# Kernel optimization log

Measured on AMD Instinct MI355X. Metric: run time of the kernel, lower is better.

## Reference

```python
import jax, jax.numpy as jnp
import numpy as np

B, S, E = 1, 8192, 1024

def setup_inputs() -> dict:
    key = jax.random.key(0)
    ks = jax.random.split(key, 7)
    scale = 1.0 / np.sqrt(E)
    q = jax.random.normal(ks[0], (B, S, E), dtype=jnp.float32)
    Wq = jax.random.uniform(ks[1], (E, E), jnp.float32, -scale, scale)
    bq = jax.random.uniform(ks[2], (E,), jnp.float32, -scale, scale)
    Wk = jax.random.uniform(ks[3], (E, E), jnp.float32, -scale, scale)
    bk = jax.random.uniform(ks[4], (E,), jnp.float32, -scale, scale)
    Wv = jax.random.uniform(ks[5], (E, E), jnp.float32, -scale, scale)
    bv = jax.random.uniform(ks[6], (E,), jnp.float32, -scale, scale)
    return {"q": q, "Wq": Wq, "bq": bq, "Wk": Wk, "bk": bk, "Wv": Wv, "bv": bv}

def reference(q, Wq, bq, Wk, bk, Wv, bv):
    # k and v default to q in the original module
    Q = jnp.einsum('bse,fe->bsf', q, Wq) + bq          # [B,S,E]
    K = jnp.einsum('bse,fe->bsf', q, Wk) + bk          # [B,S,E]
    V = jnp.einsum('bse,fe->bsf', q, Wv) + bv          # [B,S,E]
    weights = jax.nn.softmax(K, axis=1)                # softmax over sequence dim
    # sum over seq -> [B,E], then sum over E keepdim -> [B,1] (faithful to source)
    weighted_context = jnp.sum(weights * V, axis=1).sum(axis=1, keepdims=True)
    Y = jax.nn.sigmoid(Q) * weighted_context           # broadcast (valid since B==1)
    return Y
```

## Files before the change

### kernel.cpp

```cpp
#include <hip/hip_runtime.h>
#include <hip/hip_bf16.h>
#include <stdint.h>

typedef __bf16 bf16_t;
typedef __bf16 bf16x8 __attribute__((ext_vector_type(8)));
typedef float f32x4 __attribute__((ext_vector_type(4)));

#define NKT 16

__device__ __forceinline__ void gload_lds16(const void* g, void* l) {
  using gptr_t = const __attribute__((address_space(1))) void*;
  using lptr_t = __attribute__((address_space(3))) void*;
  gptr_t gp = (gptr_t)(uintptr_t)g;
  lptr_t lp = (lptr_t)(uint32_t)(uintptr_t)l;
  __builtin_amdgcn_global_load_lds(gp, lp, 16, 0, 0);
}

__device__ __forceinline__ bf16x8 cvt8v(const float* __restrict__ src, int i8) {
  const float4* s = reinterpret_cast<const float4*>(src) + (size_t)i8 * 2;
  float4 a = s[0], b = s[1];
  bf16x8 o;
  o[0] = (bf16_t)a.x; o[1] = (bf16_t)a.y; o[2] = (bf16_t)a.z; o[3] = (bf16_t)a.w;
  o[4] = (bf16_t)b.x; o[5] = (bf16_t)b.y; o[6] = (bf16_t)b.z; o[7] = (bf16_t)b.w;
  return o;
}

__global__ __launch_bounds__(256) void cvt_all(const float* __restrict__ q,
                                               const float* __restrict__ Wk,
                                               const float* __restrict__ Wv,
                                               const float* __restrict__ Wq,
                                               const float* __restrict__ bk,
                                               const float* __restrict__ bv,
                                               bf16_t* __restrict__ qb,
                                               bf16_t* __restrict__ Wkv,
                                               bf16_t* __restrict__ Wqb,
                                               float* __restrict__ bkv) {
  const int b = blockIdx.x;
  const int t = threadIdx.x;
  if (b < 4096) {
    int i = b * 256 + t;
    *reinterpret_cast<bf16x8*>(qb + (size_t)i * 8) = cvt8v(q, i);
  } else if (b < 4608) {
    int i = (b - 4096) * 256 + t;
    int j = i >> 7, c8 = i & 127;
    *reinterpret_cast<bf16x8*>(Wkv + (size_t)j * 2048 + c8 * 8) = cvt8v(Wk, i);
  } else if (b < 5120) {
    int i = (b - 4608) * 256 + t;
    int j = i >> 7, c8 = i & 127;
    *reinterpret_cast<bf16x8*>(Wkv + (size_t)j * 2048 + 1024 + c8 * 8) = cvt8v(Wv, i);
  } else if (b < 5632) {
    int i = (b - 5120) * 256 + t;
    *reinterpret_cast<bf16x8*>(Wqb + (size_t)i * 8) = cvt8v(Wq, i);
  } else {
#pragma unroll
    for (int u = 0; u < 4; ++u) {
      int j = t * 4 + u;
      bkv[2 * j] = bk[j];
      bkv[2 * j + 1] = bv[j];
    }
  }
}

__global__ __launch_bounds__(512, 1) void gemm_kv8(const bf16_t* __restrict__ A,
                                                   const bf16_t* __restrict__ Bkv,
                                                   const float* __restrict__ bkv,
                                                   float* __restrict__ pden,
                                                   float* __restrict__ pnum) {
  __shared__ bf16_t lA[2 * 256 * 64];
  __shared__ bf16_t lB[2 * 256 * 64];
  __shared__ float sD[2][128];
  __shared__ float sN[2][128];

  const int tid = threadIdx.x;
  const int w = tid >> 6, l = tid & 63;
  const int wr = w >> 2, wc = w & 3;
  const int swz = (blockIdx.x & 7) * 32 + (blockIdx.x >> 3);
  const int bx = swz & 7, by = swz >> 3;
  const int m0 = by * 256, n0 = bx * 256;

  const int rl3 = l >> 3;
  const int scol = ((l & 7) ^ rl3) * 8;
  const int fr = l & 15, fg = l >> 4, sw = l & 7;

  const bf16_t* Ab = A + (size_t)(m0 + w * 8 + rl3) * 1024 + scol;
  const bf16_t* Bb = Bkv + (size_t)(n0 + w * 8 + rl3) * 1024 + scol;

  f32x4 acc[8][4];
#pragma unroll
  for (int m = 0; m < 8; ++m)
#pragma unroll
    for (int n = 0; n < 4; ++n) acc[m][n] = (f32x4){0.f, 0.f, 0.f, 0.f};

#define STAGE_A(kt, h, r, slot)                                              \
  gload_lds16(Ab + (size_t)((h) * 128 + (r) * 64) * 1024 + (kt) * 64,        \
              &lA[(slot) * 16384 + ((h) * 128 + (r) * 64 + w * 8) * 64])
#define STAGE_B(kt, h, r, slot)                                              \
  gload_lds16(Bb + (size_t)((h) * 128 + (r) * 64) * 1024 + (kt) * 64,        \
              &lB[(slot) * 16384 + ((h) * 128 + (r) * 64 + w * 8) * 64])
#define RD_A(mm, ks) \
  (*reinterpret_cast<const bf16x8*>(&lA[aBase + ((mm) * 16 + fr) * 64 + ((((ks) * 4) + fg) ^ sw) * 8]))
#define RD_B(nn, ks) \
  (*reinterpret_cast<const bf16x8*>(&lB[bBase + ((nn) * 16 + fr) * 64 + ((((ks) * 4) + fg) ^ sw) * 8]))

  STAGE_A(0, 0, 0, 0); STAGE_A(0, 0, 1, 0); STAGE_A(0, 1, 0, 0); STAGE_A(0, 1, 1, 0);
  STAGE_B(0, 0, 0, 0); STAGE_B(0, 0, 1, 0); STAGE_B(0, 1, 0, 0); STAGE_B(0, 1, 1, 0);

#pragma unroll 1
  for (int T = 0; T < NKT; ++T) {
    const int slot = T & 1, ns = slot ^ 1;
    const bool pf = (T + 1) < NKT;
    if (pf) { STAGE_A(T + 1, 0, 0, ns); STAGE_A(T + 1, 0, 1, ns); }
    if (pf) asm volatile("s_waitcnt vmcnt(2)" ::: "memory");
    else    asm volatile("s_waitcnt vmcnt(0)" ::: "memory");
    __builtin_amdgcn_s_barrier();
    __builtin_amdgcn_sched_barrier(0);

    const int aBase = slot * 16384 + wr * 8192;
    const int bBase = slot * 16384 + wc * 4096;
    bf16x8 af[4], bfv[4];
#pragma unroll
    for (int n = 0; n < 4; ++n) bfv[n] = RD_B(n, 0);
#pragma unroll
    for (int m = 0; m < 4; ++m) af[m] = RD_A(m, 0);
    if (pf) { STAGE_A(T + 1, 1, 0, ns); STAGE_A(T + 1, 1, 1, ns); }
    __builtin_amdgcn_s_setprio(1);
#pragma unroll
    for (int m = 0; m < 4; ++m)
#pragma unroll
      for (int n = 0; n < 4; ++n)
        acc[m][n] = __builtin_amdgcn_mfma_f32_16x16x32_bf16(af[m], bfv[n], acc[m][n], 0, 0, 0);
    __builtin_amdgcn_s_setprio(0);
    __builtin_amdgcn_s_barrier();
    __builtin_amdgcn_sched_barrier(0);
#pragma unroll
    for (int m = 0; m < 4; ++m) af[m] = RD_A(m + 4, 0);
    if (pf) { STAGE_B(T + 1, 0, 0, ns); STAGE_B(T + 1, 0, 1, ns); }
    __builtin_amdgcn_s_setprio(1);
#pragma unroll
    for (int m = 0; m < 4; ++m)
#pragma unroll
      for (int n = 0; n < 4; ++n)
        acc[m + 4][n] = __builtin_amdgcn_mfma_f32_16x16x32_bf16(af[m], bfv[n], acc[m + 4][n], 0, 0, 0);
    __builtin_amdgcn_s_setprio(0);
    __builtin_amdgcn_s_barrier();
    __builtin_amdgcn_sched_barrier(0);
#pragma unroll
    for (int n = 0; n < 4; ++n) bfv[n] = RD_B(n, 1);
#pragma unroll
    for (int m = 0; m < 4; ++m) af[m] = RD_A(m, 1);
    if (pf) { STAGE_B(T + 1, 1, 0, ns); STAGE_B(T + 1, 1, 1, ns); }
    __builtin_amdgcn_s_setprio(1);
#pragma unroll
    for (int m = 0; m < 4; ++m)
#pragma unroll
      for (int n = 0; n < 4; ++n)
        acc[m][n] = __builtin_amdgcn_mfma_f32_16x16x32_bf16(af[m], bfv[n], acc[m][n], 0, 0, 0);
    __builtin_amdgcn_s_setprio(0);
    __builtin_amdgcn_s_barrier();
    __builtin_amdgcn_sched_barrier(0);
#pragma unroll
    for (int m = 0; m < 4; ++m) af[m] = RD_A(m + 4, 1);
    __builtin_amdgcn_s_setprio(1);
#pragma unroll
    for (int m = 0; m < 4; ++m)
#pragma unroll
      for (int n = 0; n < 4; ++n)
        acc[m + 4][n] = __builtin_amdgcn_mfma_f32_16x16x32_bf16(af[m], bfv[n], acc[m + 4][n], 0, 0, 0);
    __builtin_amdgcn_s_setprio(0);
    __builtin_amdgcn_s_barrier();
    __builtin_amdgcn_sched_barrier(0);
  }

  float dpn[4] = {0.f, 0.f, 0.f, 0.f};
  float npn[4] = {0.f, 0.f, 0.f, 0.f};
#pragma unroll
  for (int n = 0; n < 4; ++n) {
    const int col = n0 + wc * 64 + n * 16 + fr;
    const float bc = bkv[col];
#pragma unroll
    for (int m = 0; m < 8; ++m)
#pragma unroll
      for (int r = 0; r < 4; ++r) {
        float x = acc[m][n][r] + bc;
        float xp = __shfl_xor(x, 1);
        float e = __expf(x);
        dpn[n] += e;
        npn[n] += e * xp;
      }
    dpn[n] += __shfl_xor(dpn[n], 16); dpn[n] += __shfl_xor(dpn[n], 32);
    npn[n] += __shfl_xor(npn[n], 16); npn[n] += __shfl_xor(npn[n], 32);
  }
  if (l < 16 && (l & 1) == 0) {
#pragma unroll
    for (int n = 0; n < 4; ++n) {
      sD[wr][wc * 32 + n * 8 + (l >> 1)] = dpn[n];
      sN[wr][wc * 32 + n * 8 + (l >> 1)] = npn[n];
    }
  }
  __syncthreads();
  if (tid < 128) {
    pden[(size_t)by * 1024 + bx * 128 + tid] = sD[0][tid] + sD[1][tid];
    pnum[(size_t)by * 1024 + bx * 128 + tid] = sN[0][tid] + sN[1][tid];
  }
#undef STAGE_A
#undef STAGE_B
#undef RD_A
#undef RD_B
}

__global__ __launch_bounds__(1024) void finalize(const float* __restrict__ pden,
                                                 const float* __restrict__ pnum,
                                                 float* __restrict__ cval) {
  const int t = threadIdx.x;
  float d = 0.f, nm = 0.f;
  for (int b = 0; b < 32; ++b) {
    d += pden[b * 1024 + t];
    nm += pnum[b * 1024 + t];
  }
  float val = nm / d;
  __shared__ float red[1024];
  red[t] = val;
  __syncthreads();
  for (int s = 512; s > 0; s >>= 1) {
    if (t < s) red[t] += red[t + s];
    __syncthreads();
  }
  if (t == 0) cval[0] = red[0];
}

__global__ __launch_bounds__(512, 1) void gemm_q8(const bf16_t* __restrict__ A,
                                                  const bf16_t* __restrict__ Bq,
                                                  const float* __restrict__ bias,
                                                  const float* __restrict__ cptr,
                                                  float* __restrict__ C) {
  __shared__ bf16_t lA[2 * 256 * 64];
  __shared__ bf16_t lB[2 * 128 * 64];

  const int tid = threadIdx.x;
  const int w = tid >> 6, l = tid & 63;
  const int wr = w >> 1, wc = w & 1;
  const int swz = (blockIdx.x & 7) * 32 + (blockIdx.x >> 3);
  const int bx = swz & 7, by = swz >> 3;
  const int m0 = by * 256, n0 = bx * 128;

  const int rl3 = l >> 3;
  const int scol = ((l & 7) ^ rl3) * 8;
  const int fr = l & 15, fg = l >> 4, sw = l & 7;

  const bf16_t* Ab = A + (size_t)(m0 + w * 8 + rl3) * 1024 + scol;
  const bf16_t* Bb = Bq + (size_t)(n0 + w * 8 + rl3) * 1024 + scol;

  f32x4 acc[4][4];
#pragma unroll
  for (int m = 0; m < 4; ++m)
#pragma unroll
    for (int n = 0; n < 4; ++n) acc[m][n] = (f32x4){0.f, 0.f, 0.f, 0.f};

#define STAGE_A(kt, h, r, slot)                                              \
  gload_lds16(Ab + (size_t)((h) * 128 + (r) * 64) * 1024 + (kt) * 64,        \
              &lA[(slot) * 16384 + ((h) * 128 + (r) * 64 + w * 8) * 64])
#define STAGE_B(kt, h, slot)                                                 \
  gload_lds16(Bb + (size_t)((h) * 64) * 1024 + (kt) * 64,                    \
              &lB[(slot) * 8192 + ((h) * 64 + w * 8) * 64])
#define RD_A(mm, ks) \
  (*reinterpret_cast<const bf16x8*>(&lA[aBase + ((mm) * 16 + fr) * 64 + ((((ks) * 4) + fg) ^ sw) * 8]))
#define RD_B(nn, ks) \
  (*reinterpret_cast<const bf16x8*>(&lB[bBase + ((nn) * 16 + fr) * 64 + ((((ks) * 4) + fg) ^ sw) * 8]))

  STAGE_A(0, 0, 0, 0); STAGE_A(0, 0, 1, 0); STAGE_A(0, 1, 0, 0); STAGE_A(0, 1, 1, 0);
  STAGE_B(0, 0, 0); STAGE_B(0, 1, 0);

#pragma unroll 1
  for (int T = 0; T < NKT; ++T) {
    const int slot = T & 1, ns = slot ^ 1;
    const bool pf = (T + 1) < NKT;
    if (pf) { STAGE_A(T + 1, 0, 0, ns); STAGE_A(T + 1, 0, 1, ns); }
    if (pf) asm volatile("s_waitcnt vmcnt(2)" ::: "memory");
    else    asm volatile("s_waitcnt vmcnt(0)" ::: "memory");
    __builtin_amdgcn_s_barrier();
    __builtin_amdgcn_sched_barrier(0);

    const int aBase = slot * 16384 + wr * 4096;
    const int bBase = slot * 8192 + wc * 4096;
    bf16x8 af[2], bfv[4];
#pragma unroll
    for (int n = 0; n < 4; ++n) bfv[n] = RD_B(n, 0);
    af[0] = RD_A(0, 0); af[1] = RD_A(1, 0);
    if (pf) { STAGE_A(T + 1, 1, 0, ns); STAGE_A(T + 1, 1, 1, ns); }
    __builtin_amdgcn_s_setprio(1);
#pragma unroll
    for (int m = 0; m < 2; ++m)
#pragma unroll
      for (int n = 0; n < 4; ++n)
        acc[m][n] = __builtin_amdgcn_mfma_f32_16x16x32_bf16(af[m], bfv[n], acc[m][n], 0, 0, 0);
    __builtin_amdgcn_s_setprio(0);
    __builtin_amdgcn_s_barrier();
    __builtin_amdgcn_sched_barrier(0);
    af[0] = RD_A(2, 0); af[1] = RD_A(3, 0);
    if (pf) STAGE_B(T + 1, 0, ns);
    __builtin_amdgcn_s_setprio(1);
#pragma unroll
    for (int m = 0; m < 2; ++m)
#pragma unroll
      for (int n = 0; n < 4; ++n)
        acc[m + 2][n] = __builtin_amdgcn_mfma_f32_16x16x32_bf16(af[m], bfv[n], acc[m + 2][n], 0, 0, 0);
    __builtin_amdgcn_s_setprio(0);
    __builtin_amdgcn_s_barrier();
    __builtin_amdgcn_sched_barrier(0);
#pragma unroll
    for (int n = 0; n < 4; ++n) bfv[n] = RD_B(n, 1);
    af[0] = RD_A(0, 1); af[1] = RD_A(1, 1);
    if (pf) STAGE_B(T + 1, 1, ns);
    __builtin_amdgcn_s_setprio(1);
#pragma unroll
    for (int m = 0; m < 2; ++m)
#pragma unroll
      for (int n = 0; n < 4; ++n)
        acc[m][n] = __builtin_amdgcn_mfma_f32_16x16x32_bf16(af[m], bfv[n], acc[m][n], 0, 0, 0);
    __builtin_amdgcn_s_setprio(0);
    __builtin_amdgcn_s_barrier();
    __builtin_amdgcn_sched_barrier(0);
    af[0] = RD_A(2, 1); af[1] = RD_A(3, 1);
    __builtin_amdgcn_s_setprio(1);
#pragma unroll
    for (int m = 0; m < 2; ++m)
#pragma unroll
      for (int n = 0; n < 4; ++n)
        acc[m + 2][n] = __builtin_amdgcn_mfma_f32_16x16x32_bf16(af[m], bfv[n], acc[m + 2][n], 0, 0, 0);
    __builtin_amdgcn_s_setprio(0);
    __builtin_amdgcn_s_barrier();
    __builtin_amdgcn_sched_barrier(0);
  }

  const float cv = cptr[0];
#pragma unroll
  for (int n = 0; n < 4; ++n) {
    const int col = n0 + wc * 64 + n * 16 + fr;
    const float bs = bias[col];
#pragma unroll
    for (int m = 0; m < 4; ++m) {
      const int row = m0 + wr * 64 + m * 16 + fg * 4;
#pragma unroll
      for (int r = 0; r < 4; ++r) {
        float v = acc[m][n][r] + bs;
        v = cv / (1.f + __expf(-v));
        C[(size_t)(row + r) * 1024 + col] = v;
      }
    }
  }
#undef STAGE_A
#undef STAGE_B
#undef RD_A
#undef RD_B
}

extern "C" void kernel_launch(void* const* d_in, const int* in_sizes, int n_in,
                              void* d_out, int out_size, void* d_ws, size_t ws_size,
                              hipStream_t stream) {
  const float* q = (const float*)d_in[0];
  const float* Wq = (const float*)d_in[1];
  const float* bq = (const float*)d_in[2];
  const float* Wk = (const float*)d_in[3];
  const float* bk = (const float*)d_in[4];
  const float* Wv = (const float*)d_in[5];
  const float* bv = (const float*)d_in[6];
  float* out = (float*)d_out;

  char* ws = (char*)d_ws;
  bf16_t* qb = (bf16_t*)ws;
  bf16_t* Wkv = (bf16_t*)(ws + (size_t)16 * 1024 * 1024);
  bf16_t* Wqb = (bf16_t*)(ws + (size_t)20 * 1024 * 1024);
  float* bkv = (float*)(ws + (size_t)22 * 1024 * 1024);
  float* pden = (float*)(ws + (size_t)23 * 1024 * 1024);
  float* pnum = (float*)(ws + (size_t)23 * 1024 * 1024 + 131072);
  float* cval = (float*)(ws + (size_t)23 * 1024 * 1024 + 262144);

  cvt_all<<<5633, 256, 0, stream>>>(q, Wk, Wv, Wq, bk, bv, qb, Wkv, Wqb, bkv);
  gemm_kv8<<<256, 512, 0, stream>>>(qb, Wkv, bkv, pden, pnum);
  finalize<<<1, 1024, 0, stream>>>(pden, pnum, cval);
  gemm_q8<<<256, 512, 0, stream>>>(qb, Wqb, bq, cval, out);
}
```

Before: 77.84 us.

## Fuse KV GEMM, finalize and Q GEMM into one persistent kernel with grid barrier

Merges the KV GEMM, the single-block finalize reduction and the Q GEMM into one kernel of 256 blocks. Each block publishes its softmax partials, increments an atomic counter, computes its Q tile while other blocks finish, then spins until all 256 have arrived and reduces the partials itself. This removes two kernel launches and the serial one-block finalize, and hides the barrier wait behind the Q GEMM. In exchange it relies on all 256 blocks being co-resident, adds a memset, and has every block redundantly read all partials; the spin is capped, so a missed arrival would give wrong results rather than hang.

```diff
diff --git a/kernel.cpp b/kernel.cpp
--- a/kernel.cpp
+++ b/kernel.cpp
@@ -61,35 +61,44 @@
   }
 }
 
-__global__ __launch_bounds__(512, 1) void gemm_kv8(const bf16_t* __restrict__ A,
+__global__ __launch_bounds__(512, 1) void aft_mega(const bf16_t* __restrict__ A,
                                                    const bf16_t* __restrict__ Bkv,
+                                                   const bf16_t* __restrict__ Bq,
                                                    const float* __restrict__ bkv,
+                                                   const float* __restrict__ bq,
                                                    float* __restrict__ pden,
-                                                   float* __restrict__ pnum) {
+                                                   float* __restrict__ pnum,
+                                                   int* __restrict__ bar,
+                                                   float* __restrict__ out) {
   __shared__ bf16_t lA[2 * 256 * 64];
   __shared__ bf16_t lB[2 * 256 * 64];
   __shared__ float sD[2][128];
   __shared__ float sN[2][128];
+  __shared__ float red[512];
 
   const int tid = threadIdx.x;
   const int w = tid >> 6, l = tid & 63;
-  const int wr = w >> 2, wc = w & 3;
   const int swz = (blockIdx.x & 7) * 32 + (blockIdx.x >> 3);
   const int bx = swz & 7, by = swz >> 3;
-  const int m0 = by * 256, n0 = bx * 256;
+  const int m0 = by * 256;
 
   const int rl3 = l >> 3;
   const int scol = ((l & 7) ^ rl3) * 8;
   const int fr = l & 15, fg = l >> 4, sw = l & 7;
 
-  const bf16_t* Ab = A + (size_t)(m0 + w * 8 + rl3) * 1024 + scol;
-  const bf16_t* Bb = Bkv + (size_t)(n0 + w * 8 + rl3) * 1024 + scol;
-
-  f32x4 acc[8][4];
-#pragma unroll
-  for (int m = 0; m < 8; ++m)
-#pragma unroll
-    for (int n = 0; n < 4; ++n) acc[m][n] = (f32x4){0.f, 0.f, 0.f, 0.f};
+  const bf16_t* Abase = A + (size_t)(m0 + w * 8 + rl3) * 1024 + scol;
+
+  {
+    const int kwr = w >> 2, kwc = w & 3;
+    const int n0 = bx * 256;
+    const bf16_t* Ab = Abase;
+    const bf16_t* Bb = Bkv + (size_t)(n0 + w * 8 + rl3) * 1024 + scol;
+
+    f32x4 acc[8][4];
+#pragma unroll
+    for (int m = 0; m < 8; ++m)
+#pragma unroll
+      for (int n = 0; n < 4; ++n) acc[m][n] = (f32x4){0.f, 0.f, 0.f, 0.f};
 
 #define STAGE_A(kt, h, r, slot)                                              \
   gload_lds16(Ab + (size_t)((h) * 128 + (r) * 64) * 1024 + (kt) * 64,        \
@@ -102,159 +111,128 @@
 #define RD_B(nn, ks) \
   (*reinterpret_cast<const bf16x8*>(&lB[bBase + ((nn) * 16 + fr) * 64 + ((((ks) * 4) + fg) ^ sw) * 8]))
 
-  STAGE_A(0, 0, 0, 0); STAGE_A(0, 0, 1, 0); STAGE_A(0, 1, 0, 0); STAGE_A(0, 1, 1, 0);
-  STAGE_B(0, 0, 0, 0); STAGE_B(0, 0, 1, 0); STAGE_B(0, 1, 0, 0); STAGE_B(0, 1, 1, 0);
+    STAGE_A(0, 0, 0, 0); STAGE_A(0, 0, 1, 0); STAGE_A(0, 1, 0, 0); STAGE_A(0, 1, 1, 0);
+    STAGE_B(0, 0, 0, 0); STAGE_B(0, 0, 1, 0); STAGE_B(0, 1, 0, 0); STAGE_B(0, 1, 1, 0);
 
 #pragma unroll 1
-  for (int T = 0; T < NKT; ++T) {
-    const int slot = T & 1, ns = slot ^ 1;
-    const bool pf = (T + 1) < NKT;
-    if (pf) { STAGE_A(T + 1, 0, 0, ns); STAGE_A(T + 1, 0, 1, ns); }
-    if (pf) asm volatile("s_waitcnt vmcnt(2)" ::: "memory");
-    else    asm volatile("s_waitcnt vmcnt(0)" ::: "memory");
-    __builtin_amdgcn_s_barrier();
-    __builtin_amdgcn_sched_barrier(0);
-
-    const int aBase = slot * 16384 + wr * 8192;
-    const int bBase = slot * 16384 + wc * 4096;
-    bf16x8 af[4], bfv[4];
-#pragma unroll
-    for (int n = 0; n < 4; ++n) bfv[n] = RD_B(n, 0);
-#pragma unroll
-    for (int m = 0; m < 4; ++m) af[m] = RD_A(m, 0);
-    if (pf) { STAGE_A(T + 1, 1, 0, ns); STAGE_A(T + 1, 1, 1, ns); }
-    __builtin_amdgcn_s_setprio(1);
-#pragma unroll
-    for (int m = 0; m < 4; ++m)
-#pragma unroll
-      for (int n = 0; n < 4; ++n)
-        acc[m][n] = __builtin_amdgcn_mfma_f32_16x16x32_bf16(af[m], bfv[n], acc[m][n], 0, 0, 0);
-    __builtin_amdgcn_s_setprio(0);
-    __builtin_amdgcn_s_barrier();
-    __builtin_amdgcn_sched_barrier(0);
-#pragma unroll
-    for (int m = 0; m < 4; ++m) af[m] = RD_A(m + 4, 0);
-    if (pf) { STAGE_B(T + 1, 0, 0, ns); STAGE_B(T + 1, 0, 1, ns); }
-    __builtin_amdgcn_s_setprio(1);
-#pragma unroll
-    for (int m = 0; m < 4; ++m)
-#pragma unroll
-      for (int n = 0; n < 4; ++n)
-        acc[m + 4][n] = __builtin_amdgcn_mfma_f32_16x16x32_bf16(af[m], bfv[n], acc[m + 4][n], 0, 0, 0);
-    __builtin_amdgcn_s_setprio(0);
-    __builtin_amdgcn_s_barrier();
-    __builtin_amdgcn_sched_barrier(0);
-#pragma unroll
-    for (int n = 0; n < 4; ++n) bfv[n] = RD_B(n, 1);
-#pragma unroll
-    for (int m = 0; m < 4; ++m) af[m] = RD_A(m, 1);
-    if (pf) { STAGE_B(T + 1, 1, 0, ns); STAGE_B(T + 1, 1, 1, ns); }
-    __builtin_amdgcn_s_setprio(1);
-#pragma unroll
-    for (int m = 0; m < 4; ++m)
-#pragma unroll
-      for (int n = 0; n < 4; ++n)
-        acc[m][n] = __builtin_amdgcn_mfma_f32_16x16x32_bf16(af[m], bfv[n], acc[m][n], 0, 0, 0);
-    __builtin_amdgcn_s_setprio(0);
-    __builtin_amdgcn_s_barrier();
-    __builtin_amdgcn_sched_barrier(0);
-#pragma unroll
-    for (int m = 0; m < 4; ++m) af[m] = RD_A(m + 4, 1);
-    __builtin_amdgcn_s_setprio(1);
-#pragma unroll
-    for (int m = 0; m < 4; ++m)
-#pragma unroll
-      for (int n = 0; n < 4; ++n)
-        acc[m + 4][n] = __builtin_amdgcn_mfma_f32_16x16x32_bf16(af[m], bfv[n], acc[m + 4][n], 0, 0, 0);
-    __builtin_amdgcn_s_setprio(0);
-    __builtin_amdgcn_s_barrier();
-    __builtin_amdgcn_sched_barrier(0);
-  }
-
-  float dpn[4] = {0.f, 0.f, 0.f, 0.f};
-  float npn[4] = {0.f, 0.f, 0.f, 0.f};
-#pragma unroll
-  for (int n = 0; n < 4; ++n) {
-    const int col = n0 + wc * 64 + n * 16 + fr;
-    const float bc = bkv[col];
-#pragma unroll
-    for (int m = 0; m < 8; ++m)
-#pragma unroll
-      for (int r = 0; r < 4; ++r) {
-        float x = acc[m][n][r] + bc;
-        float xp = __shfl_xor(x, 1);
-        float e = __expf(x);
-        dpn[n] += e;
-        npn[n] += e * xp;
-      }
-    dpn[n] += __shfl_xor(dpn[n], 16); dpn[n] += __shfl_xor(dpn[n], 32);
-    npn[n] += __shfl_xor(npn[n], 16); npn[n] += __shfl_xor(npn[n], 32);
-  }
-  if (l < 16 && (l & 1) == 0) {
-#pragma unroll
-    for (int n = 0; n < 4; ++n) {
-      sD[wr][wc * 32 + n * 8 + (l >> 1)] = dpn[n];
-      sN[wr][wc * 32 + n * 8 + (l >> 1)] = npn[n];
-    }
-  }
-  __syncthreads();
-  if (tid < 128) {
-    pden[(size_t)by * 1024 + bx * 128 + tid] = sD[0][tid] + sD[1][tid];
-    pnum[(size_t)by * 1024 + bx * 128 + tid] = sN[0][tid] + sN[1][tid];
-  }
+    for (int T = 0; T < NKT; ++T) {
+      const int slot = T & 1, ns = slot ^ 1;
+      const bool pf = (T + 1) < NKT;
+      if (pf) { STAGE_A(T + 1, 0, 0, ns); STAGE_A(T + 1, 0, 1, ns); }
+      if (pf) asm volatile("s_waitcnt vmcnt(2)" ::: "memory");
+      else    asm volatile("s_waitcnt vmcnt(0)" ::: "memory");
+      __builtin_amdgcn_s_barrier();
+      __builtin_amdgcn_sched_barrier(0);
+
+      const int aBase = slot * 16384 + kwr * 8192;
+      const int bBase = slot * 16384 + kwc * 4096;
+      bf16x8 af[4], bfv[4];
+#pragma unroll
+      for (int n = 0; n < 4; ++n) bfv[n] = RD_B(n, 0);
+#pragma unroll
+      for (int m = 0; m < 4; ++m) af[m] = RD_A(m, 0);
+      if (pf) { STAGE_A(T + 1, 1, 0, ns); STAGE_A(T + 1, 1, 1, ns); }
+      __builtin_amdgcn_s_setprio(1);
+#pragma unroll
+      for (int m = 0; m < 4; ++m)
+#pragma unroll
+        for (int n = 0; n < 4; ++n)
+          acc[m][n] = __builtin_amdgcn_mfma_f32_16x16x32_bf16(af[m], bfv[n], acc[m][n], 0, 0, 0);
+      __builtin_amdgcn_s_setprio(0);
+      __builtin_amdgcn_s_barrier();
+      __builtin_amdgcn_sched_barrier(0);
+#pragma unroll
+      for (int m = 0; m < 4; ++m) af[m] = RD_A(m + 4, 0);
+      if (pf) { STAGE_B(T + 1, 0, 0, ns); STAGE_B(T + 1, 0, 1, ns); }
+      __builtin_amdgcn_s_setprio(1);
+#pragma unroll
+      for (int m = 0; m < 4; ++m)
+#pragma unroll
+        for (int n = 0; n < 4; ++n)
+          acc[m + 4][n] = __builtin_amdgcn_mfma_f32_16x16x32_bf16(af[m], bfv[n], acc[m + 4][n], 0, 0, 0);
+      __builtin_amdgcn_s_setprio(0);
+      __builtin_amdgcn_s_barrier();
+      __builtin_amdgcn_sched_barrier(0);
+#pragma unroll
+      for (int n = 0; n < 4; ++n) bfv[n] = RD_B(n, 1);
+#pragma unroll
+      for (int m = 0; m < 4; ++m) af[m] = RD_A(m, 1);
+      if (pf) { STAGE_B(T + 1, 1, 0, ns); STAGE_B(T + 1, 1, 1, ns); }
+      __builtin_amdgcn_s_setprio(1);
+#pragma unroll
+      for (int m = 0; m < 4; ++m)
+#pragma unroll
+        for (int n = 0; n < 4; ++n)
+          acc[m][n] = __builtin_amdgcn_mfma_f32_16x16x32_bf16(af[m], bfv[n], acc[m][n], 0, 0, 0);
+      __builtin_amdgcn_s_setprio(0);
+      __builtin_amdgcn_s_barrier();
+      __builtin_amdgcn_sched_barrier(0);
+#pragma unroll
+      for (int m = 0; m < 4; ++m) af[m] = RD_A(m + 4, 1);
+      __builtin_amdgcn_s_setprio(1);
+#pragma unroll
+      for (int m = 0; m < 4; ++m)
+#pragma unroll
+        for (int n = 0; n < 4; ++n)
+          acc[m + 4][n] = __builtin_amdgcn_mfma_f32_16x16x32_bf16(af[m], bfv[n], acc[m + 4][n], 0, 0, 0);
+      __builtin_amdgcn_s_setprio(0);
+      __builtin_amdgcn_s_barrier();
+      __builtin_amdgcn_sched_barrier(0);
+    }
 #undef STAGE_A
 #undef STAGE_B
 #undef RD_A
 #undef RD_B
-}
-
-__global__ __launch_bounds__(1024) void finalize(const float* __restrict__ pden,
-                                                 const float* __restrict__ pnum,
-                                                 float* __restrict__ cval) {
-  const int t = threadIdx.x;
-  float d = 0.f, nm = 0.f;
-  for (int b = 0; b < 32; ++b) {
-    d += pden[b * 1024 + t];
-    nm += pnum[b * 1024 + t];
-  }
-  float val = nm / d;
-  __shared__ float red[1024];
-  red[t] = val;
+
+    float dpn[4] = {0.f, 0.f, 0.f, 0.f};
+    float npn[4] = {0.f, 0.f, 0.f, 0.f};
+#pragma unroll
+    for (int n = 0; n < 4; ++n) {
+      const int col = n0 + kwc * 64 + n * 16 + fr;
+      const float bc = bkv[col];
+#pragma unroll
+      for (int m = 0; m < 8; ++m)
+#pragma unroll
+        for (int r = 0; r < 4; ++r) {
+          float x = acc[m][n][r] + bc;
+          float xp = __shfl_xor(x, 1);
+          float e = __expf(x);
+          dpn[n] += e;
+          npn[n] += e * xp;
+        }
+      dpn[n] += __shfl_xor(dpn[n], 16); dpn[n] += __shfl_xor(dpn[n], 32);
+      npn[n] += __shfl_xor(npn[n], 16); npn[n] += __shfl_xor(npn[n], 32);
+    }
+    if (l < 16 && (l & 1) == 0) {
+#pragma unroll
+      for (int n = 0; n < 4; ++n) {
+        sD[kwr][kwc * 32 + n * 8 + (l >> 1)] = dpn[n];
+        sN[kwr][kwc * 32 + n * 8 + (l >> 1)] = npn[n];
+      }
+    }
+    __syncthreads();
+    if (tid < 128) {
+      pden[(size_t)by * 1024 + bx * 128 + tid] = sD[0][tid] + sD[1][tid];
+      pnum[(size_t)by * 1024 + bx * 128 + tid] = sN[0][tid] + sN[1][tid];
+    }
+  }
   __syncthreads();
-  for (int s = 512; s > 0; s >>= 1) {
-    if (t < s) red[t] += red[t + s];
-    __syncthreads();
-  }
-  if (t == 0) cval[0] = red[0];
-}
-
-__global__ __launch_bounds__(512, 1) void gemm_q8(const bf16_t* __restrict__ A,
-                                                  const bf16_t* __restrict__ Bq,
-                                                  const float* __restrict__ bias,
-                                                  const float* __restrict__ cptr,
-                                                  float* __restrict__ C) {
-  __shared__ bf16_t lA[2 * 256 * 64];
-  __shared__ bf16_t lB[2 * 128 * 64];
-
-  const int tid = threadIdx.x;
-  const int w = tid >> 6, l = tid & 63;
-  const int wr = w >> 1, wc = w & 1;
-  const int swz = (blockIdx.x & 7) * 32 + (blockIdx.x >> 3);
-  const int bx = swz & 7, by = swz >> 3;
-  const int m0 = by * 256, n0 = bx * 128;
-
-  const int rl3 = l >> 3;
-  const int scol = ((l & 7) ^ rl3) * 8;
-  const int fr = l & 15, fg = l >> 4, sw = l & 7;
-
-  const bf16_t* Ab = A + (size_t)(m0 + w * 8 + rl3) * 1024 + scol;
-  const bf16_t* Bb = Bq + (size_t)(n0 + w * 8 + rl3) * 1024 + scol;
-
-  f32x4 acc[4][4];
+  if (tid == 0) {
+    __threadfence();
+    atomicAdd(bar, 1);
+  }
+
+  f32x4 qacc[4][4];
 #pragma unroll
   for (int m = 0; m < 4; ++m)
 #pragma unroll
-    for (int n = 0; n < 4; ++n) acc[m][n] = (f32x4){0.f, 0.f, 0.f, 0.f};
+    for (int n = 0; n < 4; ++n) qacc[m][n] = (f32x4){0.f, 0.f, 0.f, 0.f};
+
+  {
+    const int qwr = w >> 1, qwc = w & 1;
+    const int n0 = bx * 128;
+    const bf16_t* Ab = Abase;
+    const bf16_t* Bb = Bq + (size_t)(n0 + w * 8 + rl3) * 1024 + scol;
 
 #define STAGE_A(kt, h, r, slot)                                              \
   gload_lds16(Ab + (size_t)((h) * 128 + (r) * 64) * 1024 + (kt) * 64,        \
@@ -267,91 +245,124 @@
 #define RD_B(nn, ks) \
   (*reinterpret_cast<const bf16x8*>(&lB[bBase + ((nn) * 16 + fr) * 64 + ((((ks) * 4) + fg) ^ sw) * 8]))
 
-  STAGE_A(0, 0, 0, 0); STAGE_A(0, 0, 1, 0); STAGE_A(0, 1, 0, 0); STAGE_A(0, 1, 1, 0);
-  STAGE_B(0, 0, 0); STAGE_B(0, 1, 0);
+    STAGE_A(0, 0, 0, 0); STAGE_A(0, 0, 1, 0); STAGE_A(0, 1, 0, 0); STAGE_A(0, 1, 1, 0);
+    STAGE_B(0, 0, 0); STAGE_B(0, 1, 0);
 
 #pragma unroll 1
-  for (int T = 0; T < NKT; ++T) {
-    const int slot = T & 1, ns = slot ^ 1;
-    const bool pf = (T + 1) < NKT;
-    if (pf) { STAGE_A(T + 1, 0, 0, ns); STAGE_A(T + 1, 0, 1, ns); }
-    if (pf) asm volatile("s_waitcnt vmcnt(2)" ::: "memory");
-    else    asm volatile("s_waitcnt vmcnt(0)" ::: "memory");
-    __builtin_amdgcn_s_barrier();
-    __builtin_amdgcn_sched_barrier(0);
-
-    const int aBase = slot * 16384 + wr * 4096;
-    const int bBase = slot * 8192 + wc * 4096;
-    bf16x8 af[2], bfv[4];
-#pragma unroll
-    for (int n = 0; n < 4; ++n) bfv[n] = RD_B(n, 0);
-    af[0] = RD_A(0, 0); af[1] = RD_A(1, 0);
-    if (pf) { STAGE_A(T + 1, 1, 0, ns); STAGE_A(T + 1, 1, 1, ns); }
-    __builtin_amdgcn_s_setprio(1);
-#pragma unroll
-    for (int m = 0; m < 2; ++m)
-#pragma unroll
-      for (int n = 0; n < 4; ++n)
-        acc[m][n] = __builtin_amdgcn_mfma_f32_16x16x32_bf16(af[m], bfv[n], acc[m][n], 0, 0, 0);
-    __builtin_amdgcn_s_setprio(0);
-    __builtin_amdgcn_s_barrier();
-    __builtin_amdgcn_sched_barrier(0);
-    af[0] = RD_A(2, 0); af[1] = RD_A(3, 0);
-    if (pf) STAGE_B(T + 1, 0, ns);
-    __builtin_amdgcn_s_setprio(1);
-#pragma unroll
-    for (int m = 0; m < 2; ++m)
-#pragma unroll
-      for (int n = 0; n < 4; ++n)
-        acc[m + 2][n] = __builtin_amdgcn_mfma_f32_16x16x32_bf16(af[m], bfv[n], acc[m + 2][n], 0, 0, 0);
-    __builtin_amdgcn_s_setprio(0);
-    __builtin_amdgcn_s_barrier();
-    __builtin_amdgcn_sched_barrier(0);
-#pragma unroll
-    for (int n = 0; n < 4; ++n) bfv[n] = RD_B(n, 1);
-    af[0] = RD_A(0, 1); af[1] = RD_A(1, 1);
-    if (pf) STAGE_B(T + 1, 1, ns);
-    __builtin_amdgcn_s_setprio(1);
-#pragma unroll
-    for (int m = 0; m < 2; ++m)
-#pragma unroll
-      for (int n = 0; n < 4; ++n)
-        acc[m][n] = __builtin_amdgcn_mfma_f32_16x16x32_bf16(af[m], bfv[n], acc[m][n], 0, 0, 0);
-    __builtin_amdgcn_s_setprio(0);
-    __builtin_amdgcn_s_barrier();
-    __builtin_amdgcn_sched_barrier(0);
-    af[0] = RD_A(2, 1); af[1] = RD_A(3, 1);
-    __builtin_amdgcn_s_setprio(1);
-#pragma unroll
-    for (int m = 0; m < 2; ++m)
-#pragma unroll
-      for (int n = 0; n < 4; ++n)
-        acc[m + 2][n] = __builtin_amdgcn_mfma_f32_16x16x32_bf16(af[m], bfv[n], acc[m + 2][n], 0, 0, 0);
-    __builtin_amdgcn_s_setprio(0);
-    __builtin_amdgcn_s_barrier();
-    __builtin_amdgcn_sched_barrier(0);
-  }
-
-  const float cv = cptr[0];
-#pragma unroll
-  for (int n = 0; n < 4; ++n) {
-    const int col = n0 + wc * 64 + n * 16 + fr;
-    const float bs = bias[col];
-#pragma unroll
-    for (int m = 0; m < 4; ++m) {
-      const int row = m0 + wr * 64 + m * 16 + fg * 4;
-#pragma unroll
-      for (int r = 0; r < 4; ++r) {
-        float v = acc[m][n][r] + bs;
-        v = cv / (1.f + __expf(-v));
-        C[(size_t)(row + r) * 1024 + col] = v;
-      }
-    }
-  }
+    for (int T = 0; T < NKT; ++T) {
+      const int slot = T & 1, ns = slot ^ 1;
+      const bool pf = (T + 1) < NKT;
+      if (pf) { STAGE_A(T + 1, 0, 0, ns); STAGE_A(T + 1, 0, 1, ns); }
+      if (pf) asm volatile("s_waitcnt vmcnt(2)" ::: "memory");
+      else    asm volatile("s_waitcnt vmcnt(0)" ::: "memory");
+      __builtin_amdgcn_s_barrier();
+      __builtin_amdgcn_sched_barrier(0);
+
+      const int aBase = slot * 16384 + qwr * 4096;
+      const int bBase = slot * 8192 + qwc * 4096;
+      bf16x8 af[2], bfv[4];
+#pragma unroll
+      for (int n = 0; n < 4; ++n) bfv[n] = RD_B(n, 0);
+      af[0] = RD_A(0, 0); af[1] = RD_A(1, 0);
+      if (pf) { STAGE_A(T + 1, 1, 0, ns); STAGE_A(T + 1, 1, 1, ns); }
+      __builtin_amdgcn_s_setprio(1);
+#pragma unroll
+      for (int m = 0; m < 2; ++m)
+#pragma unroll
+        for (int n = 0; n < 4; ++n)
+          qacc[m][n] = __builtin_amdgcn_mfma_f32_16x16x32_bf16(af[m], bfv[n], qacc[m][n], 0, 0, 0);
+      __builtin_amdgcn_s_setprio(0);
+      __builtin_amdgcn_s_barrier();
+      __builtin_amdgcn_sched_barrier(0);
+      af[0] = RD_A(2, 0); af[1] = RD_A(3, 0);
+      if (pf) STAGE_B(T + 1, 0, ns);
+      __builtin_amdgcn_s_setprio(1);
+#pragma unroll
+      for (int m = 0; m < 2; ++m)
+#pragma unroll
+        for (int n = 0; n < 4; ++n)
+          qacc[m + 2][n] = __builtin_amdgcn_mfma_f32_16x16x32_bf16(af[m], bfv[n], qacc[m + 2][n], 0, 0, 0);
+      __builtin_amdgcn_s_setprio(0);
+      __builtin_amdgcn_s_barrier();
+      __builtin_amdgcn_sched_barrier(0);
+#pragma unroll
+      for (int n = 0; n < 4; ++n) bfv[n] = RD_B(n, 1);
+      af[0] = RD_A(0, 1); af[1] = RD_A(1, 1);
+      if (pf) STAGE_B(T + 1, 1, ns);
+      __builtin_amdgcn_s_setprio(1);
+#pragma unroll
+      for (int m = 0; m < 2; ++m)
+#pragma unroll
+        for (int n = 0; n < 4; ++n)
+          qacc[m][n] = __builtin_amdgcn_mfma_f32_16x16x32_bf16(af[m], bfv[n], qacc[m][n], 0, 0, 0);
+      __builtin_amdgcn_s_setprio(0);
+      __builtin_amdgcn_s_barrier();
+      __builtin_amdgcn_sched_barrier(0);
+      af[0] = RD_A(2, 1); af[1] = RD_A(3, 1);
+      __builtin_amdgcn_s_setprio(1);
+#pragma unroll
+      for (int m = 0; m < 2; ++m)
+#pragma unroll
+        for (int n = 0; n < 4; ++n)
+          qacc[m + 2][n] = __builtin_amdgcn_mfma_f32_16x16x32_bf16(af[m], bfv[n], qacc[m + 2][n], 0, 0, 0);
+      __builtin_amdgcn_s_setprio(0);
+      __builtin_amdgcn_s_barrier();
+      __builtin_amdgcn_sched_barrier(0);
+    }
 #undef STAGE_A
 #undef STAGE_B
 #undef RD_A
 #undef RD_B
+  }
+
+  if (tid == 0) {
+    int spins = 0;
+    while (__hip_atomic_load(bar, __ATOMIC_ACQUIRE, __HIP_MEMORY_SCOPE_AGENT) < 256) {
+      if (++spins > (1 << 22)) break;
+    }
+    __threadfence();
+  }
+  __syncthreads();
+
+  float vsum = 0.f;
+#pragma unroll
+  for (int j = 0; j < 2; ++j) {
+    const int c = tid + j * 512;
+    float d = 0.f, nm = 0.f;
+#pragma unroll 8
+    for (int b2 = 0; b2 < 32; ++b2) {
+      d += pden[b2 * 1024 + c];
+      nm += pnum[b2 * 1024 + c];
+    }
+    vsum += nm / d;
+  }
+  red[tid] = vsum;
+  __syncthreads();
+  for (int s = 256; s > 0; s >>= 1) {
+    if (tid < s) red[tid] += red[tid + s];
+    __syncthreads();
+  }
+  const float cv = red[0];
+
+  {
+    const int qwr = w >> 1, qwc = w & 1;
+    const int n0 = bx * 128;
+#pragma unroll
+    for (int n = 0; n < 4; ++n) {
+      const int col = n0 + qwc * 64 + n * 16 + fr;
+      const float bs = bq[col];
+#pragma unroll
+      for (int m = 0; m < 4; ++m) {
+        const int row = m0 + qwr * 64 + m * 16 + fg * 4;
+#pragma unroll
+        for (int r = 0; r < 4; ++r) {
+          float v = qacc[m][n][r] + bs;
+          v = cv / (1.f + __expf(-v));
+          out[(size_t)(row + r) * 1024 + col] = v;
+        }
+      }
+    }
+  }
 }
 
 extern "C" void kernel_launch(void* const* d_in, const int* in_sizes, int n_in,
@@ -373,10 +384,9 @@
   float* bkv = (float*)(ws + (size_t)22 * 1024 * 1024);
   float* pden = (float*)(ws + (size_t)23 * 1024 * 1024);
   float* pnum = (float*)(ws + (size_t)23 * 1024 * 1024 + 131072);
-  float* cval = (float*)(ws + (size_t)23 * 1024 * 1024 + 262144);
-
+  int* bar = (int*)(ws + (size_t)23 * 1024 * 1024 + 262144);
+
+  hipMemsetAsync(bar, 0, 4, stream);
   cvt_all<<<5633, 256, 0, stream>>>(q, Wk, Wv, Wq, bk, bv, qb, Wkv, Wqb, bkv);
-  gemm_kv8<<<256, 512, 0, stream>>>(qb, Wkv, bkv, pden, pnum);
-  finalize<<<1, 1024, 0, stream>>>(pden, pnum, cval);
-  gemm_q8<<<256, 512, 0, stream>>>(qb, Wqb, bq, cval, out);
-}
+  aft_mega<<<256, 512, 0, stream>>>(qb, Wkv, Wqb, bkv, bq, pden, pnum, bar, out);
+}
```

After: 93.22 us. 19.8% more time.
